# Performance work log

Measured on AMD Instinct MI355X. Metric: run time of the kernel, lower is better.

The kernel has to match this reference:

```python
import jax, jax.numpy as jnp
import numpy as np

KERNEL_MUL = 2.0
KERNEL_NUM = 5


def setup_inputs() -> dict:
    key = jax.random.key(0)
    k1, k2 = jax.random.split(key)
    source = jax.random.normal(k1, (4096, 512), dtype=jnp.float32)
    target = jax.random.normal(k2, (4096, 512), dtype=jnp.float32)
    return {"source": source, "target": target}


def reference(source, target):
    B = source.shape[0]
    src = source.reshape(B, -1)
    tgt = target.reshape(B, -1)
    total = jnp.concatenate([src, tgt], axis=0)  # [2B, D]
    n = 2 * B

    # Pairwise squared L2 via ||a||^2 + ||b||^2 - 2 a.b (GEMM trick)
    sq = jnp.sum(total * total, axis=-1)  # [2B]
    d2 = sq[:, None] + sq[None, :] - 2.0 * (total @ total.T)  # [2B, 2B]
    d2 = jnp.maximum(d2, 0.0)

    # Median-heuristic-style bandwidth; torch uses L2_distance.data (no grad)
    bandwidth = jax.lax.stop_gradient(jnp.sum(d2)) / (n * n - n)
    bandwidth = bandwidth / (KERNEL_MUL ** (KERNEL_NUM // 2))

    # Multi-bandwidth Gaussian kernel sum
    kernels = jnp.zeros_like(d2)
    for i in range(KERNEL_NUM):
        kernels = kernels + jnp.exp(-d2 / (bandwidth * (KERNEL_MUL ** i)))

    XX = kernels[:B, :B]
    YY = kernels[B:, B:]
    XY = kernels[:B, B:]
    YX = kernels[B:, :B]
    return jnp.mean(XX + YY - XY - YX)
```

## Files before the change

kernel.cpp:

```cpp
#include <hip/hip_runtime.h>


typedef int i32x4 __attribute__((ext_vector_type(4)));

#define N_TOT  8192
#define DIM    512
#define QSCALE 24.0f
#define NSLAB  128
#define NBLK   1088
#define NWAVE  4352
#define FP_OFF 295040
#define IMG_OFF 327680ULL

__device__ __forceinline__ int q8(float x) {
    int q = __float2int_rn(x * QSCALE);
    return max(-127, min(127, q));
}

__device__ __forceinline__ void gload16(const void* g, void* l) {
    __builtin_amdgcn_global_load_lds(
        (const __attribute__((address_space(1))) unsigned int*)g,
        (__attribute__((address_space(3))) unsigned int*)l, 16, 0, 0);
}

__global__ __launch_bounds__(256) void k_pre(
    const float* __restrict__ src, const float* __restrict__ tgt,
    unsigned char* __restrict__ img,
    float* __restrict__ sq, float* __restrict__ v)
{
    __shared__ __align__(16) signed char qt[128][80];
    const int b = blockIdx.x;
    const int p = b >> 3, kp = b & 7;
    const int t = threadIdx.x;
    const float* base = ((p < 32) ? src + (size_t)p * 128 * DIM
                                  : tgt + (size_t)(p - 32) * 128 * DIM) + kp * 64;
    {
        int r = t >> 1, ch = (t & 1) * 32;
        const float* qp = base + (size_t)r * DIM + ch;
        float rsq = 0.f;
        #pragma unroll
        for (int j = 0; j < 8; ++j) {
            float4 x = *(const float4*)(qp + j * 4);
            int q0 = q8(x.x), q1 = q8(x.y), q2 = q8(x.z), q3 = q8(x.w);
            unsigned int w = (q0 & 255) | ((q1 & 255) << 8) | ((q2 & 255) << 16)
                             | ((unsigned)(q3 & 255) << 24);
            *(unsigned int*)&qt[r][ch + j * 4] = w;
            rsq += (float)(q0 * q0 + q1 * q1 + q2 * q2 + q3 * q3);
        }
        rsq += __shfl_xor(rsq, 1);
        if ((t & 1) == 0) atomicAdd(&sq[p * 128 + r], rsq);
    }
    __syncthreads();
    #pragma unroll
    for (int h = 0; h < 2; ++h) {
        int ci = t + h * 256;
        int g = ci >> 6, lane = ci & 63;
        int row = g * 16 + (lane & 15), c0 = (lane >> 4) * 16;
        uint4 w = *(const uint4*)&qt[row][c0];
        *(uint4*)(img + (size_t)p * 65536 + (size_t)kp * 8192
                  + (size_t)g * 1024 + (size_t)lane * 16) = w;
    }
    if (t < 64) {
        float s = 0.f;
        for (int r = 0; r < 128; ++r) s += (float)qt[r][t];
        atomicAdd(&v[kp * 64 + t], s);
    }
}

#define LA(BUF, KP)                                                  \
    do {                                                             \
        BUF[0] = *(const i32x4*)(lA + (KP) * 4096 + lofs);           \
        BUF[1] = *(const i32x4*)(lA + (KP) * 4096 + 1024 + lofs);    \
        BUF[2] = *(const i32x4*)(lA + (KP) * 4096 + 2048 + lofs);    \
        BUF[3] = *(const i32x4*)(lA + (KP) * 4096 + 3072 + lofs);    \
    } while (0)

#define LB(BUF, KP)                                                  \
    do {                                                             \
        BUF[0] = *(const i32x4*)(pB + (KP) * 8192 + lofs);           \
        BUF[1] = *(const i32x4*)(pB + (KP) * 8192 + 1024 + lofs);    \
        BUF[2] = *(const i32x4*)(pB + (KP) * 8192 + 2048 + lofs);    \
        BUF[3] = *(const i32x4*)(pB + (KP) * 8192 + 3072 + lofs);    \
    } while (0)

#define MF(A, B)                                                               \
    do {                                                                       \
        _Pragma("unroll")                                                      \
        for (int m_ = 0; m_ < 4; ++m_)                                         \
            _Pragma("unroll")                                                  \
            for (int n_ = 0; n_ < 4; ++n_)                                     \
                acc[m_][n_] = __builtin_amdgcn_mfma_i32_16x16x64_i8(           \
                    A[m_], B[n_], acc[m_][n_], 0, 0, 0);                       \
    } while (0)

__global__ __launch_bounds__(256, 3) void kmain(
    const unsigned char* __restrict__ img,
    const float* __restrict__ sq, const float* __restrict__ v,
    float* __restrict__ Fpart)
{
    __shared__ __align__(16) char lA[32768];
    __shared__ float redS[4], redV[4];

    int b = blockIdx.x;
    int s = (b & 7) * (NBLK / 8) + (b >> 3);
    int si = 0;
    while (s >= ((NSLAB - si + 7) >> 3)) { s -= (NSLAB - si + 7) >> 3; ++si; }

    const int tid  = threadIdx.x;
    const int lane = tid & 63;
    const int wid  = tid >> 6;
    const int lhi  = lane >> 4, llo = lane & 15;
    const int lofs = lane * 16;
    const char* ic = (const char*)img;
    const char* gA = ic + (size_t)(si >> 1) * 65536 + (size_t)(si & 1) * 4096;

    #pragma unroll
    for (int kp = 0; kp < 8; ++kp)
        gload16(gA + kp * 8192 + tid * 16, lA + kp * 4096 + wid * 1024);

    float Sp = 0.f;
    #pragma unroll
    for (int i = 0; i < 32; ++i) Sp += sq[tid + i * 256];
    float Vp;
    { float v0 = v[tid], v1 = v[tid + 256]; Vp = v0 * v0 + v1 * v1; }
    #pragma unroll
    for (int off = 32; off > 0; off >>= 1) {
        Sp += __shfl_down(Sp, off);
        Vp += __shfl_down(Vp, off);
    }
    if (lane == 0) { redS[wid] = Sp; redV[wid] = Vp; }
    __syncthreads();
    float S = redS[0] + redS[1] + redS[2] + redS[3];
    float V = redV[0] + redV[1] + redV[2] + redV[3];
    float sumd2 = 2.f * (float)N_TOT * S - 2.f * V;
    float bw = sumd2 / ((float)N_TOT * (float)N_TOT - (float)N_TOT) * 0.25f;
    const float c = 1.4426950408889634f / (16.f * bw);

    float local = 0.f;
    const int sj_first = si + s * 8 + wid * 2;

    #pragma unroll
    for (int pp = 0; pp < 2; ++pp) {
        const int sj = sj_first + pp;
        if (sj < NSLAB) {
            const int sjs = __builtin_amdgcn_readfirstlane(sj);
            const char* pB = ic + (size_t)(sjs >> 1) * 65536 + (size_t)(sjs & 1) * 4096;

            i32x4 acc[4][4];
            #pragma unroll
            for (int m = 0; m < 4; ++m)
                #pragma unroll
                for (int n = 0; n < 4; ++n) acc[m][n] = (i32x4){0, 0, 0, 0};

            i32x4 A0[4], A1[4], B0[4], B1[4];
            LA(A0, 0); LB(B0, 0);
            LA(A1, 1); LB(B1, 1); MF(A0, B0);
            LA(A0, 2); LB(B0, 2); MF(A1, B1);
            LA(A1, 3); LB(B1, 3); MF(A0, B0);
            LA(A0, 4); LB(B0, 4); MF(A1, B1);
            LA(A1, 5); LB(B1, 5); MF(A0, B0);
            LA(A0, 6); LB(B0, 6); MF(A1, B1);
            LA(A1, 7); LB(B1, 7); MF(A0, B0);
            MF(A1, B1);

            const float sgn  = ((si < 64) == (sj < 64)) ? 1.f : -1.f;
            const bool  diag = (si == sj);
            const float wpair = diag ? sgn : 2.f * sgn;
            float sqc_[4];
            #pragma unroll
            for (int n = 0; n < 4; ++n)
                sqc_[n] = sq[sjs * 64 + n * 16 + llo];
            float psum = 0.f;
            #pragma unroll
            for (int m = 0; m < 4; ++m) {
                float sqr_[4];
                #pragma unroll
                for (int r = 0; r < 4; ++r)
                    sqr_[r] = sq[si * 64 + m * 16 + lhi * 4 + r];
                #pragma unroll
                for (int n = 0; n < 4; ++n)
                    #pragma unroll
                    for (int r = 0; r < 4; ++r) {
                        float d2 = sqr_[r] + sqc_[n] - 2.f * (float)acc[m][n][r];
                        d2 = fmaxf(d2, 0.f);
                        float u = __builtin_amdgcn_exp2f(-d2 * c);
                        float u2 = u * u, u4 = u2 * u2, u8 = u4 * u4, u16 = u8 * u8;
                        float k5 = u + u2 + u4 + u8 + u16;
                        if (diag) {
                            int ri = m * 16 + lhi * 4 + r;
                            int cj = n * 16 + llo;
                            k5 *= (cj > ri) ? 2.f : ((cj == ri) ? 1.f : 0.f);
                        }
                        psum += k5;
                    }
            }
            local += wpair * psum;
        }
    }

    #pragma unroll
    for (int off = 32; off > 0; off >>= 1) local += __shfl_down(local, off);
    if (lane == 0) Fpart[blockIdx.x * 4 + wid] = local;
}

__global__ void k4_out(const float* __restrict__ Fpart, float* __restrict__ out) {
    int t = threadIdx.x;
    double s = 0.0;
    for (int i = t; i < NWAVE; i += 256) s += (double)Fpart[i];
    #pragma unroll
    for (int off = 32; off > 0; off >>= 1) s += __shfl_down(s, off);
    __shared__ double r[4];
    if ((t & 63) == 0) r[t >> 6] = s;
    __syncthreads();
    if (t == 0) out[0] = (float)((r[0] + r[1] + r[2] + r[3]) / ((double)4096 * 4096.0));
}

extern "C" void kernel_launch(void* const* d_in, const int* in_sizes, int n_in,
                              void* d_out, int out_size, void* d_ws, size_t ws_size,
                              hipStream_t stream) {
    const float* src = (const float*)d_in[0];
    const float* tgt = (const float*)d_in[1];
    char* ws = (char*)d_ws;
    float* sq    = (float*)ws;
    float* v     = (float*)(ws + 32768);
    float* Fpart = (float*)(ws + FP_OFF);
    unsigned char* img = (unsigned char*)(ws + IMG_OFF);
    float* out = (float*)d_out;

    hipMemsetAsync(ws, 0, 34816, stream);
    hipLaunchKernelGGL(k_pre, dim3(512), dim3(256), 0, stream, src, tgt, img, sq, v);
    hipLaunchKernelGGL(kmain, dim3(NBLK), dim3(256), 0, stream, img, sq, v, Fpart);
    hipLaunchKernelGGL(k4_out, dim3(1), dim3(256), 0, stream, Fpart, out);
}
```

Baseline: 60.09 us.

## Stage both A and B panels in LDS with persistent 256-block triangular walk

Replaces the slab-per-block scheme, where each wave read B fragments straight from global memory, with 128x128 panel tiles. Both the A and B panels are staged into LDS (128KB in total) and shared across a 2x2 wave grid. A persistent grid of 256 blocks walks contiguous runs of the upper-triangular panel pairs and reloads A only when the row panel changes. This aims to cut global traffic and improve operand reuse, at the cost of occupancy dropping to one block per CU and synchronous staging with no overlap between loads and compute.

After: 62.19 us. 1.03x slower.

```diff
diff --git a/kernel.cpp b/kernel.cpp
--- a/kernel.cpp
+++ b/kernel.cpp
@@ -6,9 +6,8 @@
 #define N_TOT  8192
 #define DIM    512
 #define QSCALE 24.0f
-#define NSLAB  128
-#define NBLK   1088
-#define NWAVE  4352
+#define NPANEL 64
+#define NPH    2080
 #define FP_OFF 295040
 #define IMG_OFF 327680ULL
 
@@ -67,56 +66,43 @@
     }
 }
 
-#define LA(BUF, KP)                                                  \
-    do {                                                             \
-        BUF[0] = *(const i32x4*)(lA + (KP) * 4096 + lofs);           \
-        BUF[1] = *(const i32x4*)(lA + (KP) * 4096 + 1024 + lofs);    \
-        BUF[2] = *(const i32x4*)(lA + (KP) * 4096 + 2048 + lofs);    \
-        BUF[3] = *(const i32x4*)(lA + (KP) * 4096 + 3072 + lofs);    \
+#define STAGEP(LDSBUF, PANEL)                                                  \
+    do {                                                                       \
+        const char* g_ = ic + (size_t)(PANEL) * 65536;                         \
+        _Pragma("unroll")                                                      \
+        for (int i_ = 0; i_ < 16; ++i_)                                        \
+            gload16(g_ + i_ * 4096 + tid * 16,                                 \
+                    LDSBUF + i_ * 4096 + wid * 1024);                          \
     } while (0)
 
-#define LB(BUF, KP)                                                  \
-    do {                                                             \
-        BUF[0] = *(const i32x4*)(pB + (KP) * 8192 + lofs);           \
-        BUF[1] = *(const i32x4*)(pB + (KP) * 8192 + 1024 + lofs);    \
-        BUF[2] = *(const i32x4*)(pB + (KP) * 8192 + 2048 + lofs);    \
-        BUF[3] = *(const i32x4*)(pB + (KP) * 8192 + 3072 + lofs);    \
-    } while (0)
-
-#define MF(A, B)                                                               \
-    do {                                                                       \
-        _Pragma("unroll")                                                      \
-        for (int m_ = 0; m_ < 4; ++m_)                                         \
-            _Pragma("unroll")                                                  \
-            for (int n_ = 0; n_ < 4; ++n_)                                     \
-                acc[m_][n_] = __builtin_amdgcn_mfma_i32_16x16x64_i8(           \
-                    A[m_], B[n_], acc[m_][n_], 0, 0, 0);                       \
-    } while (0)
-
-__global__ __launch_bounds__(256, 3) void kmain(
+__global__ __launch_bounds__(256, 1) void kmain(
     const unsigned char* __restrict__ img,
     const float* __restrict__ sq, const float* __restrict__ v,
     float* __restrict__ Fpart)
 {
-    __shared__ __align__(16) char lA[32768];
+    __shared__ __align__(16) char lA[65536];
+    __shared__ __align__(16) char lB[65536];
     __shared__ float redS[4], redV[4];
-
-    int b = blockIdx.x;
-    int s = (b & 7) * (NBLK / 8) + (b >> 3);
-    int si = 0;
-    while (s >= ((NSLAB - si + 7) >> 3)) { s -= (NSLAB - si + 7) >> 3; ++si; }
 
     const int tid  = threadIdx.x;
     const int lane = tid & 63;
     const int wid  = tid >> 6;
+    const int wr   = wid >> 1, wc = wid & 1;
     const int lhi  = lane >> 4, llo = lane & 15;
     const int lofs = lane * 16;
     const char* ic = (const char*)img;
-    const char* gA = ic + (size_t)(si >> 1) * 65536 + (size_t)(si & 1) * 4096;
-
-    #pragma unroll
-    for (int kp = 0; kp < 8; ++kp)
-        gload16(gA + kp * 8192 + tid * 16, lA + kp * 4096 + wid * 1024);
+
+    int b = blockIdx.x;
+    int s = (b & 7) * 32 + (b >> 3);
+    int p0  = s * 8 + (s < 32 ? s : 32);
+    int cnt = (s < 32) ? 9 : 8;
+
+    int rem = p0, I = 0;
+    while (rem >= NPANEL - I) { rem -= NPANEL - I; ++I; }
+    int J = I + rem;
+
+    STAGEP(lA, I);
+    STAGEP(lB, J);
 
     float Sp = 0.f;
     #pragma unroll
@@ -137,76 +123,83 @@
     const float c = 1.4426950408889634f / (16.f * bw);
 
     float local = 0.f;
-    const int sj_first = si + s * 8 + wid * 2;
-
-    #pragma unroll
-    for (int pp = 0; pp < 2; ++pp) {
-        const int sj = sj_first + pp;
-        if (sj < NSLAB) {
-            const int sjs = __builtin_amdgcn_readfirstlane(sj);
-            const char* pB = ic + (size_t)(sjs >> 1) * 65536 + (size_t)(sjs & 1) * 4096;
-
-            i32x4 acc[4][4];
+
+    for (int e = 0; e < cnt; ++e) {
+        i32x4 acc[4][4];
+        #pragma unroll
+        for (int m = 0; m < 4; ++m)
+            #pragma unroll
+            for (int n = 0; n < 4; ++n) acc[m][n] = (i32x4){0, 0, 0, 0};
+
+        #pragma unroll
+        for (int kp = 0; kp < 8; ++kp) {
+            i32x4 aF[4], bF[4];
+            #pragma unroll
+            for (int m = 0; m < 4; ++m) {
+                aF[m] = *(const i32x4*)(lA + kp * 8192 + (wr * 4 + m) * 1024 + lofs);
+                bF[m] = *(const i32x4*)(lB + kp * 8192 + (wc * 4 + m) * 1024 + lofs);
+            }
             #pragma unroll
             for (int m = 0; m < 4; ++m)
                 #pragma unroll
-                for (int n = 0; n < 4; ++n) acc[m][n] = (i32x4){0, 0, 0, 0};
-
-            i32x4 A0[4], A1[4], B0[4], B1[4];
-            LA(A0, 0); LB(B0, 0);
-            LA(A1, 1); LB(B1, 1); MF(A0, B0);
-            LA(A0, 2); LB(B0, 2); MF(A1, B1);
-            LA(A1, 3); LB(B1, 3); MF(A0, B0);
-            LA(A0, 4); LB(B0, 4); MF(A1, B1);
-            LA(A1, 5); LB(B1, 5); MF(A0, B0);
-            LA(A0, 6); LB(B0, 6); MF(A1, B1);
-            LA(A1, 7); LB(B1, 7); MF(A0, B0);
-            MF(A1, B1);
-
-            const float sgn  = ((si < 64) == (sj < 64)) ? 1.f : -1.f;
-            const bool  diag = (si == sj);
-            const float wpair = diag ? sgn : 2.f * sgn;
-            float sqc_[4];
+                for (int n = 0; n < 4; ++n)
+                    acc[m][n] = __builtin_amdgcn_mfma_i32_16x16x64_i8(
+                        aF[m], bF[n], acc[m][n], 0, 0, 0);
+        }
+
+        const float sgn  = ((I < 32) == (J < 32)) ? 1.f : -1.f;
+        const bool  diag = (I == J);
+        const float wp   = diag ? sgn : 2.f * sgn;
+        float sqc_[4];
+        #pragma unroll
+        for (int n = 0; n < 4; ++n)
+            sqc_[n] = sq[J * 128 + wc * 64 + n * 16 + llo];
+        float psum = 0.f;
+        #pragma unroll
+        for (int m = 0; m < 4; ++m) {
+            float sqr_[4];
+            #pragma unroll
+            for (int r = 0; r < 4; ++r)
+                sqr_[r] = sq[I * 128 + wr * 64 + m * 16 + lhi * 4 + r];
             #pragma unroll
             for (int n = 0; n < 4; ++n)
-                sqc_[n] = sq[sjs * 64 + n * 16 + llo];
-            float psum = 0.f;
-            #pragma unroll
-            for (int m = 0; m < 4; ++m) {
-                float sqr_[4];
                 #pragma unroll
-                for (int r = 0; r < 4; ++r)
-                    sqr_[r] = sq[si * 64 + m * 16 + lhi * 4 + r];
-                #pragma unroll
-                for (int n = 0; n < 4; ++n)
-                    #pragma unroll
-                    for (int r = 0; r < 4; ++r) {
-                        float d2 = sqr_[r] + sqc_[n] - 2.f * (float)acc[m][n][r];
-                        d2 = fmaxf(d2, 0.f);
-                        float u = __builtin_amdgcn_exp2f(-d2 * c);
-                        float u2 = u * u, u4 = u2 * u2, u8 = u4 * u4, u16 = u8 * u8;
-                        float k5 = u + u2 + u4 + u8 + u16;
-                        if (diag) {
-                            int ri = m * 16 + lhi * 4 + r;
-                            int cj = n * 16 + llo;
-                            k5 *= (cj > ri) ? 2.f : ((cj == ri) ? 1.f : 0.f);
-                        }
-                        psum += k5;
+                for (int r = 0; r < 4; ++r) {
+                    float d2 = sqr_[r] + sqc_[n] - 2.f * (float)acc[m][n][r];
+                    d2 = fmaxf(d2, 0.f);
+                    float u = __builtin_amdgcn_exp2f(-d2 * c);
+                    float u2 = u * u, u4 = u2 * u2, u8 = u4 * u4, u16 = u8 * u8;
+                    float k5 = u + u2 + u4 + u8 + u16;
+                    if (diag) {
+                        int ri = wr * 64 + m * 16 + lhi * 4 + r;
+                        int cj = wc * 64 + n * 16 + llo;
+                        k5 *= (cj > ri) ? 2.f : ((cj == ri) ? 1.f : 0.f);
                     }
-            }
-            local += wpair * psum;
-        }
+                    psum += k5;
+                }
+        }
+        local += wp * psum;
+
+        int In = I, Jn = J + 1;
+        if (Jn == NPANEL) { ++In; Jn = In; }
+        __syncthreads();
+        if (e + 1 < cnt) {
+            if (In != I) STAGEP(lA, In);
+            STAGEP(lB, Jn);
+        }
+        I = In; J = Jn;
+        __syncthreads();
     }
 
     #pragma unroll
     for (int off = 32; off > 0; off >>= 1) local += __shfl_down(local, off);
-    if (lane == 0) Fpart[blockIdx.x * 4 + wid] = local;
+    if (lane == 0) Fpart[b * 4 + wid] = local;
 }
 
 __global__ void k4_out(const float* __restrict__ Fpart, float* __restrict__ out) {
     int t = threadIdx.x;
     double s = 0.0;
-    for (int i = t; i < NWAVE; i += 256) s += (double)Fpart[i];
+    for (int i = t; i < 1024; i += 256) s += (double)Fpart[i];
     #pragma unroll
     for (int off = 32; off > 0; off >>= 1) s += __shfl_down(s, off);
     __shared__ double r[4];
@@ -229,6 +222,6 @@
 
     hipMemsetAsync(ws, 0, 34816, stream);
     hipLaunchKernelGGL(k_pre, dim3(512), dim3(256), 0, stream, src, tgt, img, sq, v);
-    hipLaunchKernelGGL(kmain, dim3(NBLK), dim3(256), 0, stream, img, sq, v, Fpart);
+    hipLaunchKernelGGL(kmain, dim3(256), dim3(256), 0, stream, img, sq, v, Fpart);
     hipLaunchKernelGGL(k4_out, dim3(1), dim3(256), 0, stream, Fpart, out);
 }
```
